# Kernel optimization log

Hardware: AMD Instinct MI355X
Metric: run time of the kernel (lower is better)

## Reference

```python
import jax, jax.numpy as jnp
import numpy as np

N = 4096

def setup_inputs() -> dict:
    key = jax.random.key(0)
    k1, k2, k3 = jax.random.split(key, 3)
    x = jax.random.normal(k1, (N, N), dtype=jnp.float32)
    # nn.Linear(N, N, bias=False) weight matrices, shape [out, in] = [N, N]
    s = 1.0 / np.sqrt(N)
    W_r = jax.random.uniform(k2, (N, N), dtype=jnp.float32, minval=-s, maxval=s)
    W_i = jax.random.uniform(k3, (N, N), dtype=jnp.float32, minval=-s, maxval=s)
    return {"x": x, "W_r": W_r, "W_i": W_i}

def reference(x, W_r, W_i):
    # Row pass: fft_in_rows[i] = Linear_real(x[i]) + 1j * Linear_imag(x[i])
    #   => R = x @ W_r^T + 1j * (x @ W_i^T)
    R_r = x @ W_r.T            # [N, N]
    R_i = x @ W_i.T            # [N, N]
    # Column pass: fft_in_cols[:, i] = fft_in_rows[:, i] @ (W_r + 1j W_i)
    #   => C = W^T @ R with W = W_r + 1j W_i (complex matmul in real arithmetic)
    C_r = W_r.T @ R_r - W_i.T @ R_i
    C_i = W_r.T @ R_i + W_i.T @ R_r
    # res = cat([real, imag], dim=1) -> [N, 2N]
    return jnp.concatenate([C_r, C_i], axis=1)
```

## Files before the change

### kernel.cpp

```cpp
#include <hip/hip_runtime.h>
#include <hip/hip_bf16.h>

#define NN 4096

typedef unsigned short u16;
using bf16x8 = __attribute__((ext_vector_type(8))) short;
using f32x4  = __attribute__((ext_vector_type(4))) float;
using u32x4  = __attribute__((ext_vector_type(4))) unsigned int;

__device__ inline u16 f2bf(float f) {
    union { float f; unsigned u; } c; c.f = f;
    unsigned r = (c.u + 0x7fffu + ((c.u >> 16) & 1u)) >> 16;
    return (u16)r;
}

__device__ inline void gld16(const void* g, void* l) {
    __builtin_amdgcn_global_load_lds(
        (const __attribute__((address_space(1))) void*)g,
        (__attribute__((address_space(3))) void*)l, 16, 0, 0);
}

__device__ inline bf16x8 negbf(bf16x8 v) {
    u32x4 u; __builtin_memcpy(&u, &v, 16);
    u ^= 0x80008000u;
    bf16x8 r; __builtin_memcpy(&r, &u, 16);
    return r;
}

__global__ __launch_bounds__(256) void cvt_bf16(const float* __restrict__ s,
                                                u16* __restrict__ d) {
    size_t i = ((size_t)blockIdx.x * 256 + threadIdx.x) * 8;
    float4 v0 = *(const float4*)(s + i);
    float4 v1 = *(const float4*)(s + i + 4);
    bf16x8 o;
    o[0] = (short)f2bf(v0.x); o[1] = (short)f2bf(v0.y);
    o[2] = (short)f2bf(v0.z); o[3] = (short)f2bf(v0.w);
    o[4] = (short)f2bf(v1.x); o[5] = (short)f2bf(v1.y);
    o[6] = (short)f2bf(v1.z); o[7] = (short)f2bf(v1.w);
    *(bf16x8*)(d + i) = o;
}

__global__ __launch_bounds__(256) void tr_cvt(const float* __restrict__ s,
                                              u16* __restrict__ d) {
    __shared__ float t[32][33];
    int x  = blockIdx.x * 32 + threadIdx.x;
    int y0 = blockIdx.y * 32;
#pragma unroll
    for (int j = 0; j < 32; j += 8)
        t[threadIdx.y + j][threadIdx.x] = s[(size_t)(y0 + threadIdx.y + j) * NN + x];
    __syncthreads();
    int x2 = blockIdx.y * 32 + threadIdx.x;
    int y2 = blockIdx.x * 32;
#pragma unroll
    for (int j = 0; j < 32; j += 8)
        d[(size_t)(y2 + threadIdx.y + j) * NN + x2] = f2bf(t[threadIdx.x][threadIdx.y + j]);
}

#define P_BAR  __builtin_amdgcn_s_barrier()
#define P_LGKM do { asm volatile("s_waitcnt lgkmcnt(0)" ::: "memory"); \
                    __builtin_amdgcn_sched_barrier(0); } while (0)
#define P_VM0  do { asm volatile("s_waitcnt vmcnt(0)" ::: "memory"); \
                    __builtin_amdgcn_sched_barrier(0); } while (0)

#define CHAIN(AF, BF, ACC) do { \
    __builtin_amdgcn_s_setprio(1); \
    _Pragma("unroll") \
    for (int i_ = 0; i_ < 4; i_++) \
        _Pragma("unroll") \
        for (int j_ = 0; j_ < 4; j_++) \
            ACC[i_][j_] = __builtin_amdgcn_mfma_f32_16x16x32_bf16(AF[i_], BF[j_], ACC[i_][j_], 0, 0, 0); \
    __builtin_amdgcn_s_setprio(0); \
} while (0)

#define RD4(DST, CC, TILE, BASE) do { \
    _Pragma("unroll") \
    for (int i_ = 0; i_ < 4; i_++) \
        DST[i_] = *(const bf16x8*)&sm[CC][TILE][((BASE) + i_ * 16 + rl) * 32 + kg]; \
} while (0)


__global__ __launch_bounds__(256, 2) void gemm_pass1(
    const u16* __restrict__ Ar, const u16* __restrict__ Ai,
    const u16* __restrict__ B,
    u16* __restrict__ Cr, u16* __restrict__ Ci) {
    __shared__ u16 sm[2][3][4096];

    const int brow = blockIdx.y * 128;
    const int bcol = blockIdx.x * 128;

    const int tid  = threadIdx.x;
    const int lane = tid & 63;
    const int wid  = tid >> 6;
    const int wm   = (wid >> 1) * 64;
    const int wn   = (wid & 1) * 64;

    f32x4 accr[4][4] = {};
    f32x4 acci[4][4] = {};

    const int r0 = tid >> 2;
    const int lb = (tid & 3) ^ ((r0 >> 1) & 3);
    const size_t aoff0 = (size_t)(brow + r0) * NN + lb * 8;
    const size_t aoff1 = aoff0 + (size_t)64 * NN;
    const size_t boff0 = (size_t)(bcol + r0) * NN + lb * 8;
    const size_t boff1 = boff0 + (size_t)64 * NN;
    const int rl = lane & 15;
    const int kg = ((lane >> 4) ^ ((rl >> 1) & 3)) * 8;

#define T0(b, kk) gld16(Ar + aoff0 + (kk), &sm[b][0][tid * 8])
#define T1(b, kk) gld16(Ar + aoff1 + (kk), &sm[b][0][2048 + tid * 8])
#define T2(b, kk) gld16(Ai + aoff0 + (kk), &sm[b][1][tid * 8])
#define T3(b, kk) gld16(Ai + aoff1 + (kk), &sm[b][1][2048 + tid * 8])
#define T4(b, kk) gld16(B  + boff0 + (kk), &sm[b][2][tid * 8])
#define T5(b, kk) gld16(B  + boff1 + (kk), &sm[b][2][2048 + tid * 8])

#define KSTEP1(CC, NB, KN, DOSTG) do { \
    bf16x8 af[4], ag[4], bb[4]; \
    RD4(af, CC, 0, wm); RD4(bb, CC, 2, wn); \
    if (DOSTG) { T0(NB, KN); T1(NB, KN); T2(NB, KN); T3(NB, KN); } \
    P_BAR; P_LGKM; \
    CHAIN(af, bb, accr); \
    RD4(ag, CC, 1, wm); \
    if (DOSTG) { T4(NB, KN); T5(NB, KN); } \
    P_BAR; P_LGKM; \
    CHAIN(ag, bb, acci); \
    if (DOSTG) P_VM0; \
    P_BAR; \
} while (0)

    T0(0, 0); T1(0, 0); T2(0, 0); T3(0, 0); T4(0, 0); T5(0, 0);
    P_VM0;
    P_BAR;
    for (int t = 0; t < NN / 32 - 1; ++t) {
        const int cc = t & 1, nb = cc ^ 1;
        KSTEP1(cc, nb, (size_t)(t + 1) * 32, 1);
    }
    KSTEP1(1, 0, 0, 0);

    const int rg = (lane >> 4) * 4;
#pragma unroll
    for (int i = 0; i < 4; i++)
#pragma unroll
        for (int j = 0; j < 4; j++) {
            int col = bcol + wn + j * 16 + rl;
#pragma unroll
            for (int r = 0; r < 4; r++) {
                int row = brow + wm + i * 16 + rg + r;
                Cr[(size_t)row * NN + col] = f2bf(accr[i][j][r]);
                Ci[(size_t)row * NN + col] = f2bf(acci[i][j][r]);
            }
        }
}

__global__ __launch_bounds__(256, 2) void gemm_pass2(
    const u16* __restrict__ Ar, const u16* __restrict__ Ai,
    const u16* __restrict__ Br, const u16* __restrict__ Bi,
    float* __restrict__ Out) {
    __shared__ u16 sm[2][4][4096];

    const int brow = blockIdx.y * 128;
    const int bcol = blockIdx.x * 128;

    const int tid  = threadIdx.x;
    const int lane = tid & 63;
    const int wid  = tid >> 6;
    const int wm   = (wid >> 1) * 64;
    const int wn   = (wid & 1) * 64;

    f32x4 accr[4][4] = {};
    f32x4 acci[4][4] = {};

    const int r0 = tid >> 2;
    const int lb = (tid & 3) ^ ((r0 >> 1) & 3);
    const size_t moff0 = (size_t)(brow + r0) * NN + lb * 8;
    const size_t moff1 = moff0 + (size_t)64 * NN;
    const size_t noff0 = (size_t)(bcol + r0) * NN + lb * 8;
    const size_t noff1 = noff0 + (size_t)64 * NN;
    const int rl = lane & 15;
    const int kg = ((lane >> 4) ^ ((rl >> 1) & 3)) * 8;

#define SL0(b, kk) gld16(Ar + moff0 + (kk), &sm[b][0][tid * 8])
#define SL1(b, kk) gld16(Ar + moff1 + (kk), &sm[b][0][2048 + tid * 8])
#define SL2(b, kk) gld16(Ai + moff0 + (kk), &sm[b][1][tid * 8])
#define SL3(b, kk) gld16(Ai + moff1 + (kk), &sm[b][1][2048 + tid * 8])
#define SL4(b, kk) gld16(Br + noff0 + (kk), &sm[b][2][tid * 8])
#define SL5(b, kk) gld16(Br + noff1 + (kk), &sm[b][2][2048 + tid * 8])
#define SL6(b, kk) gld16(Bi + noff0 + (kk), &sm[b][3][tid * 8])
#define SL7(b, kk) gld16(Bi + noff1 + (kk), &sm[b][3][2048 + tid * 8])

#define KSTEP2(CC, NB, KN, DOSTG) do { \
    bf16x8 ar[4], ai[4], br[4], bi[4]; \
     \
    RD4(ar, CC, 0, wm); RD4(bi, CC, 3, wn); \
    if (DOSTG) { SL0(NB, KN); SL1(NB, KN); SL2(NB, KN); } \
    P_BAR; P_LGKM; \
    CHAIN(ar, bi, acci); \
     \
    RD4(br, CC, 2, wn); \
    if (DOSTG) { SL3(NB, KN); SL4(NB, KN); SL5(NB, KN); } \
    P_BAR; P_LGKM; \
    CHAIN(ar, br, accr); \
     \
    RD4(ai, CC, 1, wm); \
    if (DOSTG) { SL6(NB, KN); SL7(NB, KN); } \
    P_BAR; P_LGKM; \
    CHAIN(ai, br, acci); \
     \
    _Pragma("unroll") for (int i_ = 0; i_ < 4; i_++) ai[i_] = negbf(ai[i_]); \
    CHAIN(ai, bi, accr); \
    if (DOSTG) P_VM0; \
    P_BAR; \
} while (0)

    SL0(0, 0); SL1(0, 0); SL2(0, 0); SL3(0, 0);
    SL4(0, 0); SL5(0, 0); SL6(0, 0); SL7(0, 0);
    P_VM0;
    P_BAR;
    for (int t = 0; t < NN / 32 - 1; ++t) {
        const int cc = t & 1, nb = cc ^ 1;
        KSTEP2(cc, nb, (size_t)(t + 1) * 32, 1);
    }
    KSTEP2(1, 0, 0, 0);

    const int rg = (lane >> 4) * 4;
#pragma unroll
    for (int i = 0; i < 4; i++)
#pragma unroll
        for (int j = 0; j < 4; j++) {
            int col = bcol + wn + j * 16 + rl;
#pragma unroll
            for (int r = 0; r < 4; r++) {
                int row = brow + wm + i * 16 + rg + r;
                Out[(size_t)row * (2 * NN) + col]      = accr[i][j][r];
                Out[(size_t)row * (2 * NN) + NN + col] = acci[i][j][r];
            }
        }
}

extern "C" void kernel_launch(void* const* d_in, const int* in_sizes, int n_in,
                              void* d_out, int out_size, void* d_ws, size_t ws_size,
                              hipStream_t stream) {
    const float* x  = (const float*)d_in[0];
    const float* Wr = (const float*)d_in[1];
    const float* Wi = (const float*)d_in[2];
    float* out = (float*)d_out;

    const size_t SZ = (size_t)NN * NN;
    u16* ws  = (u16*)d_ws;
    u16* xb  = ws;
    u16* Wrb = ws + SZ;
    u16* Wib = ws + 2 * SZ;
    u16* Rtr = ws + 3 * SZ;
    u16* Rti = ws + 4 * SZ;

    cvt_bf16<<<8192, 256, 0, stream>>>(x,  xb);
    cvt_bf16<<<8192, 256, 0, stream>>>(Wr, Wrb);
    cvt_bf16<<<8192, 256, 0, stream>>>(Wi, Wib);

    gemm_pass1<<<dim3(32, 32), 256, 0, stream>>>(Wrb, Wib, xb, Rtr, Rti);

    u16* WrT = xb;
    u16* WiT = Wrb;
    tr_cvt<<<dim3(128, 128), dim3(32, 8), 0, stream>>>(Wr, WrT);
    tr_cvt<<<dim3(128, 128), dim3(32, 8), 0, stream>>>(Wi, WiT);

    gemm_pass2<<<dim3(32, 32), 256, 0, stream>>>(WrT, WiT, Rtr, Rti, out);
}
```

Measured before the change: 767.5 us.

## Replace full vmcnt drains with partial waits and reorder tile loads

```diff
diff --git a/kernel.cpp b/kernel.cpp
--- a/kernel.cpp
+++ b/kernel.cpp
@@ -59,7 +59,7 @@
 #define P_BAR  __builtin_amdgcn_s_barrier()
 #define P_LGKM do { asm volatile("s_waitcnt lgkmcnt(0)" ::: "memory"); \
                     __builtin_amdgcn_sched_barrier(0); } while (0)
-#define P_VM0  do { asm volatile("s_waitcnt vmcnt(0)" ::: "memory"); \
+#define VMW(N) do { asm volatile("s_waitcnt vmcnt(" #N ")" ::: "memory"); \
                     __builtin_amdgcn_sched_barrier(0); } while (0)
 
 #define CHAIN(AF, BF, ACC) do { \
@@ -113,28 +113,26 @@
 #define T4(b, kk) gld16(B  + boff0 + (kk), &sm[b][2][tid * 8])
 #define T5(b, kk) gld16(B  + boff1 + (kk), &sm[b][2][2048 + tid * 8])
 
-#define KSTEP1(CC, NB, KN, DOSTG) do { \
+#define KSTEP1(CC, NB, KN, DOSTG, V0, V1) do { \
     bf16x8 af[4], ag[4], bb[4]; \
     RD4(af, CC, 0, wm); RD4(bb, CC, 2, wn); \
-    if (DOSTG) { T0(NB, KN); T1(NB, KN); T2(NB, KN); T3(NB, KN); } \
-    P_BAR; P_LGKM; \
+    if (DOSTG) { T0(NB, KN); T1(NB, KN); T4(NB, KN); T5(NB, KN); } \
+    VMW(V0); P_BAR; P_LGKM; \
     CHAIN(af, bb, accr); \
     RD4(ag, CC, 1, wm); \
-    if (DOSTG) { T4(NB, KN); T5(NB, KN); } \
-    P_BAR; P_LGKM; \
+    P_LGKM; \
+    if (DOSTG) { T2(NB, KN); T3(NB, KN); } \
+    VMW(V1); P_BAR; \
     CHAIN(ag, bb, acci); \
-    if (DOSTG) P_VM0; \
-    P_BAR; \
-} while (0)
-
-    T0(0, 0); T1(0, 0); T2(0, 0); T3(0, 0); T4(0, 0); T5(0, 0);
-    P_VM0;
-    P_BAR;
+} while (0)
+
+    T0(0, 0); T1(0, 0); T4(0, 0); T5(0, 0); T2(0, 0); T3(0, 0);
+    VMW(2); P_BAR;
     for (int t = 0; t < NN / 32 - 1; ++t) {
         const int cc = t & 1, nb = cc ^ 1;
-        KSTEP1(cc, nb, (size_t)(t + 1) * 32, 1);
+        KSTEP1(cc, nb, (size_t)(t + 1) * 32, 1, 4, 2);
     }
-    KSTEP1(1, 0, 0, 0);
+    KSTEP1(1, 0, 0, 0, 0, 0);
 
     const int rg = (lane >> 4) * 4;
 #pragma unroll
@@ -187,39 +185,37 @@
 #define SL6(b, kk) gld16(Bi + noff0 + (kk), &sm[b][3][tid * 8])
 #define SL7(b, kk) gld16(Bi + noff1 + (kk), &sm[b][3][2048 + tid * 8])
 
-#define KSTEP2(CC, NB, KN, DOSTG) do { \
+#define KSTEP2(CC, NB, KN, DOSTG, V0, V1, V2) do { \
     bf16x8 ar[4], ai[4], br[4], bi[4]; \
      \
     RD4(ar, CC, 0, wm); RD4(bi, CC, 3, wn); \
-    if (DOSTG) { SL0(NB, KN); SL1(NB, KN); SL2(NB, KN); } \
-    P_BAR; P_LGKM; \
+    if (DOSTG) { SL0(NB, KN); SL1(NB, KN); SL6(NB, KN); SL7(NB, KN); } \
+    VMW(V0); P_BAR; P_LGKM; \
     CHAIN(ar, bi, acci); \
      \
     RD4(br, CC, 2, wn); \
-    if (DOSTG) { SL3(NB, KN); SL4(NB, KN); SL5(NB, KN); } \
-    P_BAR; P_LGKM; \
+    P_LGKM; \
+    VMW(V1); P_BAR; \
     CHAIN(ar, br, accr); \
      \
     RD4(ai, CC, 1, wm); \
-    if (DOSTG) { SL6(NB, KN); SL7(NB, KN); } \
-    P_BAR; P_LGKM; \
+    P_LGKM; \
+    if (DOSTG) { SL4(NB, KN); SL5(NB, KN); SL2(NB, KN); SL3(NB, KN); } \
+    VMW(V2); P_BAR; \
     CHAIN(ai, br, acci); \
      \
     _Pragma("unroll") for (int i_ = 0; i_ < 4; i_++) ai[i_] = negbf(ai[i_]); \
     CHAIN(ai, bi, accr); \
-    if (DOSTG) P_VM0; \
-    P_BAR; \
-} while (0)
-
-    SL0(0, 0); SL1(0, 0); SL2(0, 0); SL3(0, 0);
-    SL4(0, 0); SL5(0, 0); SL6(0, 0); SL7(0, 0);
-    P_VM0;
-    P_BAR;
+} while (0)
+
+    SL0(0, 0); SL1(0, 0); SL6(0, 0); SL7(0, 0);
+    SL4(0, 0); SL5(0, 0); SL2(0, 0); SL3(0, 0);
+    VMW(4); P_BAR;
     for (int t = 0; t < NN / 32 - 1; ++t) {
         const int cc = t & 1, nb = cc ^ 1;
-        KSTEP2(cc, nb, (size_t)(t + 1) * 32, 1);
+        KSTEP2(cc, nb, (size_t)(t + 1) * 32, 1, 6, 4, 4);
     }
-    KSTEP2(1, 0, 0, 0);
+    KSTEP2(1, 0, 0, 0, 2, 0, 0);
 
     const int rg = (lane >> 4) * 4;
 #pragma unroll
```

Result: no change. 763.1 us (-0.6%).
